# Performance work log

Measured on AMD Instinct MI355X. Metric: run time of the kernel, lower is better.

The kernel has to match this reference:

```python
import jax, jax.numpy as jnp
import numpy as np

N, E, D, L, G = 100000, 300000, 256, 5, 4096


def _bn(x, p):
    # p: [4, dim] = (gamma, beta, running_mean, running_var); eval-mode BatchNorm1d
    g, b, m, v = p
    return (x - m) * jax.lax.rsqrt(v + 1e-5) * g + b


def setup_inputs() -> dict:
    key = jax.random.key(0)
    ks = iter(jax.random.split(key, 48))

    def nrm(shape, scale=0.02):
        return jax.random.normal(next(ks), shape, dtype=jnp.float32) * scale

    def bn_params(n, dim):
        g = 1.0 + nrm((n, dim), 0.1)
        b = nrm((n, dim), 0.1)
        m = nrm((n, dim), 0.1)
        v = 1.0 + jax.random.uniform(next(ks), (n, dim), dtype=jnp.float32)
        return jnp.stack([g, b, m, v], axis=1)  # [n,4,dim]

    return {
        "x": jax.random.randint(next(ks), (N, 9), 0, 2, dtype=jnp.int32),
        "edge_index": jax.random.randint(next(ks), (2, E), 0, N, dtype=jnp.int32),
        "edge_attr": jax.random.randint(next(ks), (E, 3), 0, 2, dtype=jnp.int32),
        "batch": jnp.sort(jax.random.randint(next(ks), (N,), 0, G, dtype=jnp.int32)),
        "atom_emb": nrm((9, 120, D)),            # AtomEncoder: 9 feature tables
        "bond_emb": nrm((L, 3, 6, D)),           # per-layer BondEncoder: 3 feature tables
        "vn0": jnp.zeros((D,), jnp.float32),     # virtualnode embedding (init 0)
        "eps": jnp.zeros((L,), jnp.float32),     # GIN eps per layer
        "conv_W1": nrm((L, D, 2 * D), 1.0 / np.sqrt(D)),     # GIN MLP (sampled BayesLinear)
        "conv_b1": nrm((L, 2 * D)),
        "conv_bn1": bn_params(L, 2 * D),
        "conv_W2": nrm((L, 2 * D, D), 1.0 / np.sqrt(2 * D)),
        "conv_b2": nrm((L, D)),
        "node_bn": bn_params(L, D),              # per-layer outer BatchNorm
        "vn_W1": nrm((L - 1, D, D), 1.0 / np.sqrt(D)),       # virtual-node MLP
        "vn_b1": nrm((L - 1, D)),
        "vn_bn1": bn_params(L - 1, D),
        "vn_W2": nrm((L - 1, D, D), 1.0 / np.sqrt(D)),
        "vn_b2": nrm((L - 1, D)),
        "vn_bn2": bn_params(L - 1, D),
    }


def reference(x, edge_index, edge_attr, batch, atom_emb, bond_emb, vn0, eps,
              conv_W1, conv_b1, conv_bn1, conv_W2, conv_b2, node_bn,
              vn_W1, vn_b1, vn_bn1, vn_W2, vn_b2, vn_bn2):
    src, dst = edge_index[0], edge_index[1]
    n_nodes = x.shape[0]
    n_layers = conv_W1.shape[0]
    # AtomEncoder: sum of 9 feature embeddings -> [N, D]
    h = atom_emb[jnp.arange(9), x].sum(axis=1)
    vn = jnp.broadcast_to(vn0, (G, vn0.shape[0]))  # [G, D]
    for l in range(n_layers):
        # broadcast virtual node into graph's nodes
        h = h + vn[batch]
        # GINConv: msg = relu(x_j + bond_emb), sum-aggregate, MLP((1+eps)x + aggr)
        e = bond_emb[l][jnp.arange(3), edge_attr].sum(axis=1)  # [E, D]
        msg = jax.nn.relu(h[src] + e)
        aggr = jax.ops.segment_sum(msg, dst, num_segments=n_nodes)
        t = (1.0 + eps[l]) * h + aggr
        t = jax.nn.relu(_bn(t @ conv_W1[l] + conv_b1[l], conv_bn1[l])) @ conv_W2[l] + conv_b2[l]
        hn = _bn(t, node_bn[l])  # outer BatchNorm (eval); dropout is identity in eval
        if l < n_layers - 1:
            hn = jax.nn.relu(hn)
            # global_add_pool of pre-conv h, then virtual-node MLP update
            vtemp = jax.ops.segment_sum(h, batch, num_segments=G) + vn
            u = jax.nn.relu(_bn(vtemp @ vn_W1[l] + vn_b1[l], vn_bn1[l]))
            vn = jax.nn.relu(_bn(u @ vn_W2[l] + vn_b2[l], vn_bn2[l]))
        h = hn
    return h  # JK == 'last'
```

## Files before the change

kernel.cpp:

```cpp
#include <hip/hip_runtime.h>

#define NN 100000
#define EE 300000
#define DD 256
#define LL 5
#define GG 4096
#define DB 512
#define MPAD 100096

typedef __attribute__((ext_vector_type(4))) float f32x4;
typedef __attribute__((ext_vector_type(8))) short s16x8;

__device__ __forceinline__ ushort f2bf(float f) {
  unsigned u = __float_as_uint(f);
  return (ushort)((u + 0x7fffu + ((u >> 16) & 1u)) >> 16);
}
__device__ __forceinline__ float b2f(ushort u) {
  return __uint_as_float(((unsigned)u) << 16);
}

__device__ __forceinline__ void gload16(const void* g, void* l) {
  __builtin_amdgcn_global_load_lds((const __attribute__((address_space(1))) void*)g,
                                   (__attribute__((address_space(3))) void*)l, 16, 0, 0);
}

__global__ void k_atom(const int* __restrict__ x, const float* __restrict__ emb,
                       ushort* __restrict__ hb) {
  int n = blockIdx.x * 4 + (threadIdx.x >> 6);
  if (n >= NN) return;
  int d = (threadIdx.x & 63) * 4;
  float ax = 0.f, ay = 0.f, az = 0.f, aw = 0.f;
#pragma unroll
  for (int f = 0; f < 9; ++f) {
    int v = x[n * 9 + f];
    const float4 t = *(const float4*)&emb[((size_t)(f * 120 + v)) * DD + d];
    ax += t.x; ay += t.y; az += t.z; aw += t.w;
  }
  ushort4 o; o.x = f2bf(ax); o.y = f2bf(ay); o.z = f2bf(az); o.w = f2bf(aw);
  *(ushort4*)&hb[(size_t)n * DD + d] = o;
}

__global__ void k_vninit(const float* __restrict__ vn0, float* __restrict__ vn) {
  int i = blockIdx.x * blockDim.x + threadIdx.x;
  if (i < GG * DD) vn[i] = vn0[i & (DD - 1)];
}

__global__ void k_goff(const int* __restrict__ batch, int* __restrict__ goff) {
  int g = blockIdx.x * blockDim.x + threadIdx.x;
  if (g > GG) return;
  if (g == GG) { goff[GG] = NN; return; }
  int lo = 0, hi = NN;
  while (lo < hi) { int mid = (lo + hi) >> 1; if (batch[mid] < g) lo = mid + 1; else hi = mid; }
  goff[g] = lo;
}

__global__ void k_zero(int* __restrict__ p, int n) {
  int i = blockIdx.x * 256 + threadIdx.x;
  if (i < n) p[i] = 0;
}

__global__ void k_deg(const int* __restrict__ dst, int* __restrict__ deg) {
  int e = blockIdx.x * 256 + threadIdx.x;
  if (e < EE) atomicAdd(&deg[dst[e]], 1);
}

__global__ void k_scan1(const int* __restrict__ deg, int* __restrict__ coff,
                        int* __restrict__ bsum) {
  __shared__ int wsum[16];
  __shared__ int wpre[16];
  int lane = threadIdx.x & 63, wid = threadIdx.x >> 6;
  int i = blockIdx.x * 1024 + threadIdx.x;
  int v = (i < NN) ? deg[i] : 0;
  int xv = v;
#pragma unroll
  for (int off = 1; off < 64; off <<= 1) {
    int y = __shfl_up(xv, off);
    if (lane >= off) xv += y;
  }
  if (lane == 63) wsum[wid] = xv;
  __syncthreads();
  if (wid == 0 && lane < 16) {
    int s = wsum[lane];
    int xx = s;
#pragma unroll
    for (int off = 1; off < 16; off <<= 1) {
      int y = __shfl_up(xx, off);
      if (lane >= off) xx += y;
    }
    wpre[lane] = xx - s;
  }
  __syncthreads();
  int val = xv + wpre[wid];
  if (i < NN) coff[i + 1] = val;
  if (threadIdx.x == 1023) bsum[blockIdx.x] = val;
}

__global__ void k_scan2(int* __restrict__ bsum, int nb) {
  __shared__ int ws[2];
  int t = threadIdx.x, lane = t & 63, wid = t >> 6;
  int v = (t < nb) ? bsum[t] : 0;
  int xv = v;
#pragma unroll
  for (int off = 1; off < 64; off <<= 1) {
    int y = __shfl_up(xv, off);
    if (lane >= off) xv += y;
  }
  if (lane == 63) ws[wid] = xv;
  __syncthreads();
  int incl = xv + ((wid == 1) ? ws[0] : 0);
  if (t < nb) bsum[t] = incl - v;
}

__global__ void k_scan3(int* __restrict__ coff, const int* __restrict__ bpre) {
  int i = blockIdx.x * 1024 + threadIdx.x;
  if (i == 0) coff[0] = 0;
  if (i < NN) coff[i + 1] += bpre[i >> 10];
}

__global__ void k_eposinit(const int* __restrict__ coff, int* __restrict__ epos) {
  int n = blockIdx.x * 256 + threadIdx.x;
  if (n < NN) epos[n] = coff[n];
}

__global__ void k_scatter(const int* __restrict__ dst, int* __restrict__ epos,
                          int* __restrict__ eid) {
  int e = blockIdx.x * 256 + threadIdx.x;
  if (e < EE) { int p = atomicAdd(&epos[dst[e]], 1); eid[p] = e; }
}

__global__ void k_sort(const int* __restrict__ coff, int* __restrict__ eid) {
  int n = blockIdx.x * 256 + threadIdx.x;
  if (n >= NN) return;
  int s = coff[n], t = coff[n + 1];
  for (int i = s + 1; i < t; ++i) {
    int key = eid[i]; int j = i - 1;
    while (j >= s && eid[j] > key) { eid[j + 1] = eid[j]; --j; }
    eid[j + 1] = key;
  }
}

__global__ void k_emeta(const int* __restrict__ eid, const int* __restrict__ srcs,
                        const int* __restrict__ eattr, unsigned* __restrict__ emeta) {
  int idx = blockIdx.x * 256 + threadIdx.x;
  if (idx >= EE) return;
  int e = eid[idx];
  int s = srcs[e];
  unsigned c = (unsigned)(eattr[e * 3 + 0] + 2 * eattr[e * 3 + 1] + 4 * eattr[e * 3 + 2]);
  emeta[idx] = (unsigned)s | (c << 17);
}

__global__ void k_bond8(const float* __restrict__ bondE, float* __restrict__ bond8) {
  int l = blockIdx.x, c = blockIdx.y, d = threadIdx.x;
  float v = bondE[(((size_t)l * 3 + 0) * 6 + (c & 1)) * DD + d]
          + bondE[(((size_t)l * 3 + 1) * 6 + ((c >> 1) & 1)) * DD + d]
          + bondE[(((size_t)l * 3 + 2) * 6 + ((c >> 2) & 1)) * DD + d];
  bond8[((size_t)l * 8 + c) * DD + d] = v;
}

__global__ void k_wt(const float* __restrict__ in, ushort* __restrict__ out, int K, int N) {
  __shared__ float t[16][17];
  int l = blockIdx.z;
  int kb = blockIdx.x * 16, nb = blockIdx.y * 16;
  int tx = threadIdx.x & 15, ty = threadIdx.x >> 4;
  t[ty][tx] = in[(size_t)l * K * N + (size_t)(kb + ty) * N + nb + tx];
  __syncthreads();
  out[(size_t)l * N * K + (size_t)(nb + ty) * K + kb + tx] = f2bf(t[tx][ty]);
}

__global__ void k_prep(const ushort* __restrict__ hb, const float* __restrict__ vn,
                       ushort* __restrict__ hvb, ushort* __restrict__ vtempb,
                       const int* __restrict__ goff, int writePool) {
  int g = blockIdx.x * 4 + (threadIdx.x >> 6);
  if (g >= GG) return;
  int d = (threadIdx.x & 63) * 4;
  float4 v = *(const float4*)&vn[(size_t)g * DD + d];
  float ax = v.x, ay = v.y, az = v.z, aw = v.w;
  int r0 = goff[g], r1 = goff[g + 1];
  for (int r = r0; r < r1; ++r) {
    ushort4 hu = *(const ushort4*)&hb[(size_t)r * DD + d];
    float h0 = b2f(hu.x) + v.x, h1 = b2f(hu.y) + v.y;
    float h2 = b2f(hu.z) + v.z, h3 = b2f(hu.w) + v.w;
    ushort4 o; o.x = f2bf(h0); o.y = f2bf(h1); o.z = f2bf(h2); o.w = f2bf(h3);
    *(ushort4*)&hvb[(size_t)r * DD + d] = o;
    ax += h0; ay += h1; az += h2; aw += h3;
  }
  if (writePool) {
    ushort4 o; o.x = f2bf(ax); o.y = f2bf(ay); o.z = f2bf(az); o.w = f2bf(aw);
    *(ushort4*)&vtempb[(size_t)g * DD + d] = o;
  }
}

__global__ void k_aggr(const ushort* __restrict__ hvb, ushort* __restrict__ tb,
                       const unsigned* __restrict__ emeta, const int* __restrict__ coff,
                       const float* __restrict__ bond8l, const float* __restrict__ epsp,
                       int l) {
  int n = blockIdx.x * 4 + (threadIdx.x >> 6);
  if (n >= NN) return;
  int d = (threadIdx.x & 63) * 4;
  float ax = 0.f, ay = 0.f, az = 0.f, aw = 0.f;
  int s0 = coff[n], s1 = coff[n + 1];
  int idx = s0;
  for (; idx + 2 <= s1; idx += 2) {
    unsigned m0 = emeta[idx], m1 = emeta[idx + 1];
    const ushort4 h0 = *(const ushort4*)&hvb[(size_t)(m0 & 0x1FFFFu) * DD + d];
    const ushort4 h1 = *(const ushort4*)&hvb[(size_t)(m1 & 0x1FFFFu) * DD + d];
    const float4 b0 = *(const float4*)&bond8l[(size_t)(m0 >> 17) * DD + d];
    const float4 b1 = *(const float4*)&bond8l[(size_t)(m1 >> 17) * DD + d];
    ax += fmaxf(b2f(h0.x) + b0.x, 0.f) + fmaxf(b2f(h1.x) + b1.x, 0.f);
    ay += fmaxf(b2f(h0.y) + b0.y, 0.f) + fmaxf(b2f(h1.y) + b1.y, 0.f);
    az += fmaxf(b2f(h0.z) + b0.z, 0.f) + fmaxf(b2f(h1.z) + b1.z, 0.f);
    aw += fmaxf(b2f(h0.w) + b0.w, 0.f) + fmaxf(b2f(h1.w) + b1.w, 0.f);
  }
  if (idx < s1) {
    unsigned m0 = emeta[idx];
    const ushort4 h0 = *(const ushort4*)&hvb[(size_t)(m0 & 0x1FFFFu) * DD + d];
    const float4 b0 = *(const float4*)&bond8l[(size_t)(m0 >> 17) * DD + d];
    ax += fmaxf(b2f(h0.x) + b0.x, 0.f);
    ay += fmaxf(b2f(h0.y) + b0.y, 0.f);
    az += fmaxf(b2f(h0.z) + b0.z, 0.f);
    aw += fmaxf(b2f(h0.w) + b0.w, 0.f);
  }
  float ep = 1.f + epsp[l];
  const ushort4 hn = *(const ushort4*)&hvb[(size_t)n * DD + d];
  ushort4 o;
  o.x = f2bf(ep * b2f(hn.x) + ax); o.y = f2bf(ep * b2f(hn.y) + ay);
  o.z = f2bf(ep * b2f(hn.z) + az); o.w = f2bf(ep * b2f(hn.w) + aw);
  *(ushort4*)&tb[(size_t)n * DD + d] = o;
}

__global__ __launch_bounds__(256) void k_mfma_gemm(
    const ushort* __restrict__ A, int M, int K,
    const ushort* __restrict__ BT, int N,
    void* __restrict__ Cv, int outBf16, int doRelu,
    const float* __restrict__ bias, const float* __restrict__ bn) {
  __shared__ ushort Asm[2][128 * 32];
  __shared__ ushort Bsm[2][128 * 32];
  const int tid = threadIdx.x;
  const int lane = tid & 63;
  const int w = tid >> 6;
  const int rowBase = blockIdx.x * 128;
  const int colBase = blockIdx.y * 128;
  const int wrow = (w >> 1) * 64, wcol = (w & 1) * 64;
  const int r16 = lane & 15, kgrp = lane >> 4;

  f32x4 acc[4][4];
#pragma unroll
  for (int m = 0; m < 4; ++m)
#pragma unroll
    for (int n = 0; n < 4; ++n) acc[m][n] = (f32x4)0.f;

  const int ca0 = tid, ca1 = tid + 256;
  const int ra0 = ca0 >> 2, ka0 = (ca0 & 3) ^ ((ra0 >> 1) & 3);
  const int ra1 = ca1 >> 2, ka1 = (ca1 & 3) ^ ((ra1 >> 1) & 3);
  const ushort* Ap0 = A + (size_t)(rowBase + ra0) * K + ka0 * 8;
  const ushort* Ap1 = A + (size_t)(rowBase + ra1) * K + ka1 * 8;
  const ushort* Bp0 = BT + (size_t)(colBase + ra0) * K + ka0 * 8;
  const ushort* Bp1 = BT + (size_t)(colBase + ra1) * K + ka1 * 8;

  int aoff[4], boff[4];
#pragma unroll
  for (int m = 0; m < 4; ++m) {
    int row = wrow + m * 16 + r16;
    aoff[m] = row * 64 + ((kgrp ^ ((row >> 1) & 3)) << 4);
    int col = wcol + m * 16 + r16;
    boff[m] = col * 64 + ((kgrp ^ ((col >> 1) & 3)) << 4);
  }

  const int nk = K >> 5;
  gload16(Ap0, (char*)Asm + ca0 * 16);
  gload16(Ap1, (char*)Asm + ca1 * 16);
  gload16(Bp0, (char*)Bsm + ca0 * 16);
  gload16(Bp1, (char*)Bsm + ca1 * 16);
  __syncthreads();

  int cur = 0;
  for (int t = 0; t < nk; ++t) {
    int nxt = cur ^ 1;
    if (t + 1 < nk) {
      int ko = (t + 1) << 5;
      gload16(Ap0 + ko, (char*)Asm + nxt * 8192 + ca0 * 16);
      gload16(Ap1 + ko, (char*)Asm + nxt * 8192 + ca1 * 16);
      gload16(Bp0 + ko, (char*)Bsm + nxt * 8192 + ca0 * 16);
      gload16(Bp1 + ko, (char*)Bsm + nxt * 8192 + ca1 * 16);
    }
    const char* cA = (const char*)Asm + cur * 8192;
    const char* cB = (const char*)Bsm + cur * 8192;
    s16x8 a[4], b[4];
#pragma unroll
    for (int m = 0; m < 4; ++m) a[m] = *(const s16x8*)(cA + aoff[m]);
#pragma unroll
    for (int n = 0; n < 4; ++n) b[n] = *(const s16x8*)(cB + boff[n]);
#pragma unroll
    for (int m = 0; m < 4; ++m)
#pragma unroll
      for (int n = 0; n < 4; ++n)
        acc[m][n] = __builtin_amdgcn_mfma_f32_16x16x32_bf16(a[m], b[n], acc[m][n], 0, 0, 0);
    __syncthreads();
    cur = nxt;
  }

  float alpha[4], beta[4];
#pragma unroll
  for (int n = 0; n < 4; ++n) {
    int col = colBase + wcol + n * 16 + r16;
    float g = bn[col], bb = bn[N + col], mm = bn[2 * N + col], vv = bn[3 * N + col];
    float s = g * rsqrtf(vv + 1e-5f);
    alpha[n] = s; beta[n] = fmaf(bias[col] - mm, s, bb);
  }
#pragma unroll
  for (int m = 0; m < 4; ++m) {
#pragma unroll
    for (int r = 0; r < 4; ++r) {
      int row = rowBase + wrow + m * 16 + kgrp * 4 + r;
      if (row < M) {
#pragma unroll
        for (int n = 0; n < 4; ++n) {
          int col = colBase + wcol + n * 16 + r16;
          float v = fmaf(acc[m][n][r], alpha[n], beta[n]);
          if (doRelu) v = fmaxf(v, 0.f);
          if (outBf16) ((ushort*)Cv)[(size_t)row * N + col] = f2bf(v);
          else         ((float*)Cv)[(size_t)row * N + col] = v;
        }
      }
    }
  }
}

extern "C" void kernel_launch(void* const* d_in, const int* in_sizes, int n_in,
                              void* d_out, int out_size, void* d_ws, size_t ws_size,
                              hipStream_t stream) {
  const int*   x     = (const int*)d_in[0];
  const int*   ei    = (const int*)d_in[1];
  const int*   ea    = (const int*)d_in[2];
  const int*   batch = (const int*)d_in[3];
  const float* atomE = (const float*)d_in[4];
  const float* bondE = (const float*)d_in[5];
  const float* vn0   = (const float*)d_in[6];
  const float* eps   = (const float*)d_in[7];
  const float* cW1   = (const float*)d_in[8];
  const float* cb1   = (const float*)d_in[9];
  const float* cbn1  = (const float*)d_in[10];
  const float* cW2   = (const float*)d_in[11];
  const float* cb2   = (const float*)d_in[12];
  const float* nbn   = (const float*)d_in[13];
  const float* vW1   = (const float*)d_in[14];
  const float* vb1   = (const float*)d_in[15];
  const float* vbn1  = (const float*)d_in[16];
  const float* vW2   = (const float*)d_in[17];
  const float* vb2   = (const float*)d_in[18];
  const float* vbn2  = (const float*)d_in[19];
  (void)in_sizes; (void)n_in; (void)out_size; (void)ws_size;

  char* wsp = (char*)d_ws;
  size_t o = 0;
  auto alloc = [&](size_t bytes) -> char* {
    char* p = wsp + o; o += (bytes + 255) & ~(size_t)255; return p;
  };
  ushort* tbuf  = (ushort*)alloc((size_t)MPAD * DD * 2);
  ushort* c1b   = (ushort*)alloc((size_t)MPAD * DB * 2);
  ushort* hb    = (ushort*)alloc((size_t)NN * DD * 2);
  float*  vn    = (float*) alloc((size_t)GG * DD * 4);
  ushort* vtmpb = (ushort*)alloc((size_t)GG * DD * 2);
  ushort* ub    = (ushort*)alloc((size_t)GG * DD * 2);
  ushort* bw1   = (ushort*)alloc((size_t)LL * DB * DD * 2);
  ushort* bw2   = (ushort*)alloc((size_t)LL * DD * DB * 2);
  ushort* bvw1  = (ushort*)alloc((size_t)(LL - 1) * DD * DD * 2);
  ushort* bvw2  = (ushort*)alloc((size_t)(LL - 1) * DD * DD * 2);
  float*  bond8 = (float*) alloc((size_t)LL * 8 * DD * 4);
  unsigned* emeta = (unsigned*)alloc((size_t)EE * 4);
  int* coff = (int*)alloc((size_t)(NN + 1) * 4);
  int* deg  = (int*)alloc((size_t)NN * 4);
  int* epos = (int*)alloc((size_t)NN * 4);
  int* eid  = (int*)alloc((size_t)EE * 4);
  int* goff = (int*)alloc((size_t)(GG + 1) * 4);
  int* bsum = (int*)alloc((size_t)128 * 4);

  const int* srcs = ei;
  const int* dsts = ei + EE;
  ushort* hvb = (ushort*)d_out;

  k_atom<<<(NN + 3) / 4, 256, 0, stream>>>(x, atomE, hb);
  k_vninit<<<(GG * DD + 255) / 256, 256, 0, stream>>>(vn0, vn);
  k_goff<<<(GG + 256) / 256, 256, 0, stream>>>(batch, goff);
  k_zero<<<(NN + 255) / 256, 256, 0, stream>>>(deg, NN);
  k_deg<<<(EE + 255) / 256, 256, 0, stream>>>(dsts, deg);
  {
    int nb = (NN + 1023) / 1024;
    k_scan1<<<nb, 1024, 0, stream>>>(deg, coff, bsum);
    k_scan2<<<1, 128, 0, stream>>>(bsum, nb);
    k_scan3<<<nb, 1024, 0, stream>>>(coff, bsum);
  }
  k_eposinit<<<(NN + 255) / 256, 256, 0, stream>>>(coff, epos);
  k_scatter<<<(EE + 255) / 256, 256, 0, stream>>>(dsts, epos, eid);
  k_sort<<<(NN + 255) / 256, 256, 0, stream>>>(coff, eid);
  k_emeta<<<(EE + 255) / 256, 256, 0, stream>>>(eid, srcs, ea, emeta);
  k_bond8<<<dim3(LL, 8), 256, 0, stream>>>(bondE, bond8);
  k_wt<<<dim3(DD / 16, DB / 16, LL), 256, 0, stream>>>(cW1, bw1, DD, DB);
  k_wt<<<dim3(DB / 16, DD / 16, LL), 256, 0, stream>>>(cW2, bw2, DB, DD);
  k_wt<<<dim3(DD / 16, DD / 16, LL - 1), 256, 0, stream>>>(vW1, bvw1, DD, DD);
  k_wt<<<dim3(DD / 16, DD / 16, LL - 1), 256, 0, stream>>>(vW2, bvw2, DD, DD);

  for (int l = 0; l < LL; ++l) {
    int writePool = (l < LL - 1) ? 1 : 0;
    k_prep<<<(GG + 3) / 4, 256, 0, stream>>>(hb, vn, hvb, vtmpb, goff, writePool);
    k_aggr<<<(NN + 3) / 4, 256, 0, stream>>>(hvb, tbuf, emeta, coff,
                                             bond8 + (size_t)l * 8 * DD, eps, l);
    k_mfma_gemm<<<dim3(MPAD / 128, DB / 128), 256, 0, stream>>>(
        tbuf, NN, DD, bw1 + (size_t)l * DB * DD, DB,
        c1b, 1, 1, cb1 + (size_t)l * DB, cbn1 + (size_t)l * 4 * DB);
    if (l < LL - 1) {
      k_mfma_gemm<<<dim3(MPAD / 128, DD / 128), 256, 0, stream>>>(
          c1b, NN, DB, bw2 + (size_t)l * DD * DB, DD,
          hb, 1, 1, cb2 + (size_t)l * DD, nbn + (size_t)l * 4 * DD);
      k_mfma_gemm<<<dim3(GG / 128, DD / 128), 256, 0, stream>>>(
          vtmpb, GG, DD, bvw1 + (size_t)l * DD * DD, DD,
          ub, 1, 1, vb1 + (size_t)l * DD, vbn1 + (size_t)l * 4 * DD);
      k_mfma_gemm<<<dim3(GG / 128, DD / 128), 256, 0, stream>>>(
          ub, GG, DD, bvw2 + (size_t)l * DD * DD, DD,
          vn, 0, 1, vb2 + (size_t)l * DD, vbn2 + (size_t)l * 4 * DD);
    } else {
      k_mfma_gemm<<<dim3(MPAD / 128, DD / 128), 256, 0, stream>>>(
          c1b, NN, DB, bw2 + (size_t)l * DD * DB, DD,
          (float*)d_out, 0, 0, cb2 + (size_t)l * DD, nbn + (size_t)l * 4 * DD);
    }
  }
}
```

Baseline: 1.154 ms.

## Fuse virtual-node broadcast into GEMM epilogue and keep full A row-tile in LDS

Removes the per-layer prep pass that re-read h and wrote h+vn. The virtual node is instead added in the atom encoder for layer 0 and in the second GIN GEMM's epilogue, after the virtual-node MLP has been reordered to run first. Pooling becomes a read-only kernel over the already-broadcast h. The GEMM is rewritten as a template that loads the whole A row tile (all of K) into LDS once and sweeps every output column chunk, streaming B double-buffered, so A is fetched from global memory only once. The trade-offs are much higher LDS use per block (fewer resident blocks), a per-row batch gather in the epilogue, and a serial loop over column chunks inside one block.

```diff
diff --git a/kernel.cpp b/kernel.cpp
--- a/kernel.cpp
+++ b/kernel.cpp
@@ -25,11 +25,12 @@
 }
 
 __global__ void k_atom(const int* __restrict__ x, const float* __restrict__ emb,
-                       ushort* __restrict__ hb) {
+                       const float* __restrict__ vn0, ushort* __restrict__ hvb) {
   int n = blockIdx.x * 4 + (threadIdx.x >> 6);
   if (n >= NN) return;
   int d = (threadIdx.x & 63) * 4;
-  float ax = 0.f, ay = 0.f, az = 0.f, aw = 0.f;
+  const float4 v0 = *(const float4*)&vn0[d];
+  float ax = v0.x, ay = v0.y, az = v0.z, aw = v0.w;
 #pragma unroll
   for (int f = 0; f < 9; ++f) {
     int v = x[n * 9 + f];
@@ -37,7 +38,7 @@
     ax += t.x; ay += t.y; az += t.z; aw += t.w;
   }
   ushort4 o; o.x = f2bf(ax); o.y = f2bf(ay); o.z = f2bf(az); o.w = f2bf(aw);
-  *(ushort4*)&hb[(size_t)n * DD + d] = o;
+  *(ushort4*)&hvb[(size_t)n * DD + d] = o;
 }
 
 __global__ void k_vninit(const float* __restrict__ vn0, float* __restrict__ vn) {
@@ -167,9 +168,8 @@
   out[(size_t)l * N * K + (size_t)(nb + ty) * K + kb + tx] = f2bf(t[tx][ty]);
 }
 
-__global__ void k_prep(const ushort* __restrict__ hb, const float* __restrict__ vn,
-                       ushort* __restrict__ hvb, ushort* __restrict__ vtempb,
-                       const int* __restrict__ goff, int writePool) {
+__global__ void k_pool(const ushort* __restrict__ hvb, const float* __restrict__ vn,
+                       ushort* __restrict__ vtempb, const int* __restrict__ goff) {
   int g = blockIdx.x * 4 + (threadIdx.x >> 6);
   if (g >= GG) return;
   int d = (threadIdx.x & 63) * 4;
@@ -177,17 +177,11 @@
   float ax = v.x, ay = v.y, az = v.z, aw = v.w;
   int r0 = goff[g], r1 = goff[g + 1];
   for (int r = r0; r < r1; ++r) {
-    ushort4 hu = *(const ushort4*)&hb[(size_t)r * DD + d];
-    float h0 = b2f(hu.x) + v.x, h1 = b2f(hu.y) + v.y;
-    float h2 = b2f(hu.z) + v.z, h3 = b2f(hu.w) + v.w;
-    ushort4 o; o.x = f2bf(h0); o.y = f2bf(h1); o.z = f2bf(h2); o.w = f2bf(h3);
-    *(ushort4*)&hvb[(size_t)r * DD + d] = o;
-    ax += h0; ay += h1; az += h2; aw += h3;
-  }
-  if (writePool) {
-    ushort4 o; o.x = f2bf(ax); o.y = f2bf(ay); o.z = f2bf(az); o.w = f2bf(aw);
-    *(ushort4*)&vtempb[(size_t)g * DD + d] = o;
-  }
+    ushort4 hu = *(const ushort4*)&hvb[(size_t)r * DD + d];
+    ax += b2f(hu.x); ay += b2f(hu.y); az += b2f(hu.z); aw += b2f(hu.w);
+  }
+  ushort4 o; o.x = f2bf(ax); o.y = f2bf(ay); o.z = f2bf(az); o.w = f2bf(aw);
+  *(ushort4*)&vtempb[(size_t)g * DD + d] = o;
 }
 
 __global__ void k_aggr(const ushort* __restrict__ hvb, ushort* __restrict__ tb,
@@ -228,101 +222,117 @@
   *(ushort4*)&tb[(size_t)n * DD + d] = o;
 }
 
-__global__ __launch_bounds__(256) void k_mfma_gemm(
-    const ushort* __restrict__ A, int M, int K,
-    const ushort* __restrict__ BT, int N,
+template<int TM, int K, int NT>
+__global__ __launch_bounds__(256) void k_gemm_f(
+    const ushort* __restrict__ A, int M,
+    const ushort* __restrict__ BT,
     void* __restrict__ Cv, int outBf16, int doRelu,
-    const float* __restrict__ bias, const float* __restrict__ bn) {
-  __shared__ ushort Asm[2][128 * 32];
-  __shared__ ushort Bsm[2][128 * 32];
+    const float* __restrict__ bias, const float* __restrict__ bn,
+    const float* __restrict__ vnAdd, const int* __restrict__ batchv) {
+  constexpr int KS = K / 8;
+  constexpr int NK = K / 32;
+  constexpr int NC = NT / 128;
+  constexpr int MF = TM / 32;
+  __shared__ ushort Alds[TM * K];
+  __shared__ ushort Blds[2][128 * 32];
   const int tid = threadIdx.x;
   const int lane = tid & 63;
   const int w = tid >> 6;
-  const int rowBase = blockIdx.x * 128;
-  const int colBase = blockIdx.y * 128;
-  const int wrow = (w >> 1) * 64, wcol = (w & 1) * 64;
+  const int rowBase = blockIdx.x * TM;
+  const int wrow = (w >> 1) * (TM / 2);
+  const int wcol = (w & 1) * 64;
   const int r16 = lane & 15, kgrp = lane >> 4;
 
-  f32x4 acc[4][4];
-#pragma unroll
-  for (int m = 0; m < 4; ++m)
+#pragma unroll
+  for (int i = 0; i < TM * KS / 256; ++i) {
+    int c = tid + i * 256;
+    int row = c / KS, s = c % KS;
+    int kg = s ^ (row & 7);
+    gload16(A + (size_t)(rowBase + row) * K + kg * 8, (char*)Alds + c * 16);
+  }
+  const int bcol0 = tid >> 2, bkg0 = (tid & 3) ^ ((bcol0 >> 1) & 3);
+  const int bcol1 = (tid + 256) >> 2, bkg1 = ((tid + 256) & 3) ^ ((bcol1 >> 1) & 3);
+  auto stageB = [&](int pc, int pt, int b) {
+    const ushort* base = BT + (size_t)pc * 128 * K + pt * 32;
+    gload16(base + (size_t)bcol0 * K + bkg0 * 8, (char*)Blds[b] + tid * 16);
+    gload16(base + (size_t)bcol1 * K + bkg1 * 8, (char*)Blds[b] + (tid + 256) * 16);
+  };
+  stageB(0, 0, 0);
+  __syncthreads();
+
+  int rbyte[MF], x7[MF];
+#pragma unroll
+  for (int m = 0; m < MF; ++m) {
+    int row = wrow + m * 16 + r16;
+    rbyte[m] = row * KS * 16;
+    x7[m] = row & 7;
+  }
+  int boff[4];
+#pragma unroll
+  for (int n = 0; n < 4; ++n) {
+    int col = wcol + n * 16 + r16;
+    boff[n] = (col * 4 + (kgrp ^ ((col >> 1) & 3))) * 16;
+  }
+
+  f32x4 acc[MF][4];
+#pragma unroll
+  for (int m = 0; m < MF; ++m)
 #pragma unroll
     for (int n = 0; n < 4; ++n) acc[m][n] = (f32x4)0.f;
 
-  const int ca0 = tid, ca1 = tid + 256;
-  const int ra0 = ca0 >> 2, ka0 = (ca0 & 3) ^ ((ra0 >> 1) & 3);
-  const int ra1 = ca1 >> 2, ka1 = (ca1 & 3) ^ ((ra1 >> 1) & 3);
-  const ushort* Ap0 = A + (size_t)(rowBase + ra0) * K + ka0 * 8;
-  const ushort* Ap1 = A + (size_t)(rowBase + ra1) * K + ka1 * 8;
-  const ushort* Bp0 = BT + (size_t)(colBase + ra0) * K + ka0 * 8;
-  const ushort* Bp1 = BT + (size_t)(colBase + ra1) * K + ka1 * 8;
-
-  int aoff[4], boff[4];
-#pragma unroll
-  for (int m = 0; m < 4; ++m) {
-    int row = wrow + m * 16 + r16;
-    aoff[m] = row * 64 + ((kgrp ^ ((row >> 1) & 3)) << 4);
-    int col = wcol + m * 16 + r16;
-    boff[m] = col * 64 + ((kgrp ^ ((col >> 1) & 3)) << 4);
-  }
-
-  const int nk = K >> 5;
-  gload16(Ap0, (char*)Asm + ca0 * 16);
-  gload16(Ap1, (char*)Asm + ca1 * 16);
-  gload16(Bp0, (char*)Bsm + ca0 * 16);
-  gload16(Bp1, (char*)Bsm + ca1 * 16);
-  __syncthreads();
-
   int cur = 0;
-  for (int t = 0; t < nk; ++t) {
-    int nxt = cur ^ 1;
-    if (t + 1 < nk) {
-      int ko = (t + 1) << 5;
-      gload16(Ap0 + ko, (char*)Asm + nxt * 8192 + ca0 * 16);
-      gload16(Ap1 + ko, (char*)Asm + nxt * 8192 + ca1 * 16);
-      gload16(Bp0 + ko, (char*)Bsm + nxt * 8192 + ca0 * 16);
-      gload16(Bp1 + ko, (char*)Bsm + nxt * 8192 + ca1 * 16);
-    }
-    const char* cA = (const char*)Asm + cur * 8192;
-    const char* cB = (const char*)Bsm + cur * 8192;
-    s16x8 a[4], b[4];
-#pragma unroll
-    for (int m = 0; m < 4; ++m) a[m] = *(const s16x8*)(cA + aoff[m]);
-#pragma unroll
-    for (int n = 0; n < 4; ++n) b[n] = *(const s16x8*)(cB + boff[n]);
-#pragma unroll
-    for (int m = 0; m < 4; ++m)
+  for (int c = 0; c < NC; ++c) {
+#pragma unroll
+    for (int t = 0; t < NK; ++t) {
+      if (t + 1 < NK) stageB(c, t + 1, cur ^ 1);
+      else if (c + 1 < NC) stageB(c + 1, 0, cur ^ 1);
+      s16x8 a[MF], b[4];
+#pragma unroll
+      for (int m = 0; m < MF; ++m)
+        a[m] = *(const s16x8*)((const char*)Alds + rbyte[m] + ((((t << 2) + kgrp) ^ x7[m]) << 4));
 #pragma unroll
       for (int n = 0; n < 4; ++n)
-        acc[m][n] = __builtin_amdgcn_mfma_f32_16x16x32_bf16(a[m], b[n], acc[m][n], 0, 0, 0);
-    __syncthreads();
-    cur = nxt;
-  }
-
-  float alpha[4], beta[4];
-#pragma unroll
-  for (int n = 0; n < 4; ++n) {
-    int col = colBase + wcol + n * 16 + r16;
-    float g = bn[col], bb = bn[N + col], mm = bn[2 * N + col], vv = bn[3 * N + col];
-    float s = g * rsqrtf(vv + 1e-5f);
-    alpha[n] = s; beta[n] = fmaf(bias[col] - mm, s, bb);
-  }
-#pragma unroll
-  for (int m = 0; m < 4; ++m) {
-#pragma unroll
-    for (int r = 0; r < 4; ++r) {
-      int row = rowBase + wrow + m * 16 + kgrp * 4 + r;
-      if (row < M) {
-#pragma unroll
-        for (int n = 0; n < 4; ++n) {
-          int col = colBase + wcol + n * 16 + r16;
-          float v = fmaf(acc[m][n][r], alpha[n], beta[n]);
-          if (doRelu) v = fmaxf(v, 0.f);
-          if (outBf16) ((ushort*)Cv)[(size_t)row * N + col] = f2bf(v);
-          else         ((float*)Cv)[(size_t)row * N + col] = v;
+        b[n] = *(const s16x8*)((const char*)Blds[cur] + boff[n]);
+#pragma unroll
+      for (int m = 0; m < MF; ++m)
+#pragma unroll
+        for (int n = 0; n < 4; ++n)
+          acc[m][n] = __builtin_amdgcn_mfma_f32_16x16x32_bf16(a[m], b[n], acc[m][n], 0, 0, 0);
+      __syncthreads();
+      cur ^= 1;
+    }
+    const int cb = c * 128;
+    float alpha[4], beta[4];
+#pragma unroll
+    for (int n = 0; n < 4; ++n) {
+      int col = cb + wcol + n * 16 + r16;
+      float g = bn[col], bb = bn[NT + col], mm = bn[2 * NT + col], vv = bn[3 * NT + col];
+      float s = g * rsqrtf(vv + 1e-5f);
+      alpha[n] = s; beta[n] = fmaf(bias[col] - mm, s, bb);
+    }
+#pragma unroll
+    for (int m = 0; m < MF; ++m) {
+#pragma unroll
+      for (int r = 0; r < 4; ++r) {
+        int row = rowBase + wrow + m * 16 + kgrp * 4 + r;
+        if (row < M) {
+          const float* vp = vnAdd ? (vnAdd + (size_t)batchv[row] * NT) : nullptr;
+#pragma unroll
+          for (int n = 0; n < 4; ++n) {
+            int col = cb + wcol + n * 16 + r16;
+            float v = fmaf(acc[m][n][r], alpha[n], beta[n]);
+            if (doRelu) v = fmaxf(v, 0.f);
+            if (vp) v += vp[col];
+            if (outBf16) ((ushort*)Cv)[(size_t)row * NT + col] = f2bf(v);
+            else         ((float*)Cv)[(size_t)row * NT + col] = v;
+          }
         }
       }
     }
+#pragma unroll
+    for (int m = 0; m < MF; ++m)
+#pragma unroll
+      for (int n = 0; n < 4; ++n) acc[m][n] = (f32x4)0.f;
   }
 }
 
@@ -358,7 +368,6 @@
   };
   ushort* tbuf  = (ushort*)alloc((size_t)MPAD * DD * 2);
   ushort* c1b   = (ushort*)alloc((size_t)MPAD * DB * 2);
-  ushort* hb    = (ushort*)alloc((size_t)NN * DD * 2);
   float*  vn    = (float*) alloc((size_t)GG * DD * 4);
   ushort* vtmpb = (ushort*)alloc((size_t)GG * DD * 2);
   ushort* ub    = (ushort*)alloc((size_t)GG * DD * 2);
@@ -379,7 +388,7 @@
   const int* dsts = ei + EE;
   ushort* hvb = (ushort*)d_out;
 
-  k_atom<<<(NN + 3) / 4, 256, 0, stream>>>(x, atomE, hb);
+  k_atom<<<(NN + 3) / 4, 256, 0, stream>>>(x, atomE, vn0, hvb);
   k_vninit<<<(GG * DD + 255) / 256, 256, 0, stream>>>(vn0, vn);
   k_goff<<<(GG + 256) / 256, 256, 0, stream>>>(batch, goff);
   k_zero<<<(NN + 255) / 256, 256, 0, stream>>>(deg, NN);
@@ -401,27 +410,28 @@
   k_wt<<<dim3(DD / 16, DD / 16, LL - 1), 256, 0, stream>>>(vW2, bvw2, DD, DD);
 
   for (int l = 0; l < LL; ++l) {
-    int writePool = (l < LL - 1) ? 1 : 0;
-    k_prep<<<(GG + 3) / 4, 256, 0, stream>>>(hb, vn, hvb, vtmpb, goff, writePool);
+    if (l < LL - 1) {
+      k_pool<<<(GG + 3) / 4, 256, 0, stream>>>(hvb, vn, vtmpb, goff);
+      k_gemm_f<64, 256, 256><<<GG / 64, 256, 0, stream>>>(
+          vtmpb, GG, bvw1 + (size_t)l * DD * DD, ub, 1, 1,
+          vb1 + (size_t)l * DD, vbn1 + (size_t)l * 4 * DD, nullptr, nullptr);
+      k_gemm_f<64, 256, 256><<<GG / 64, 256, 0, stream>>>(
+          ub, GG, bvw2 + (size_t)l * DD * DD, vn, 0, 1,
+          vb2 + (size_t)l * DD, vbn2 + (size_t)l * 4 * DD, nullptr, nullptr);
+    }
     k_aggr<<<(NN + 3) / 4, 256, 0, stream>>>(hvb, tbuf, emeta, coff,
                                              bond8 + (size_t)l * 8 * DD, eps, l);
-    k_mfma_gemm<<<dim3(MPAD / 128, DB / 128), 256, 0, stream>>>(
-        tbuf, NN, DD, bw1 + (size_t)l * DB * DD, DB,
-        c1b, 1, 1, cb1 + (size_t)l * DB, cbn1 + (size_t)l * 4 * DB);
+    k_gemm_f<128, 256, 512><<<MPAD / 128, 256, 0, stream>>>(
+        tbuf, NN, bw1 + (size_t)l * DB * DD, c1b, 1, 1,
+        cb1 + (size_t)l * DB, cbn1 + (size_t)l * 4 * DB, nullptr, nullptr);
     if (l < LL - 1) {
-      k_mfma_gemm<<<dim3(MPAD / 128, DD / 128), 256, 0, stream>>>(
-          c1b, NN, DB, bw2 + (size_t)l * DD * DB, DD,
-          hb, 1, 1, cb2 + (size_t)l * DD, nbn + (size_t)l * 4 * DD);
-      k_mfma_gemm<<<dim3(GG / 128, DD / 128), 256, 0, stream>>>(
-          vtmpb, GG, DD, bvw1 + (size_t)l * DD * DD, DD,
-          ub, 1, 1, vb1 + (size_t)l * DD, vbn1 + (size_t)l * 4 * DD);
-      k_mfma_gemm<<<dim3(GG / 128, DD / 128), 256, 0, stream>>>(
-          ub, GG, DD, bvw2 + (size_t)l * DD * DD, DD,
-          vn, 0, 1, vb2 + (size_t)l * DD, vbn2 + (size_t)l * 4 * DD);
+      k_gemm_f<64, 512, 256><<<MPAD / 64, 256, 0, stream>>>(
+          c1b, NN, bw2 + (size_t)l * DD * DB, hvb, 1, 1,
+          cb2 + (size_t)l * DD, nbn + (size_t)l * 4 * DD, vn, batch);
     } else {
-      k_mfma_gemm<<<dim3(MPAD / 128, DD / 128), 256, 0, stream>>>(
-          c1b, NN, DB, bw2 + (size_t)l * DD * DB, DD,
-          (float*)d_out, 0, 0, cb2 + (size_t)l * DD, nbn + (size_t)l * 4 * DD);
-    }
-  }
-}
+      k_gemm_f<64, 512, 256><<<MPAD / 64, 256, 0, stream>>>(
+          c1b, NN, bw2 + (size_t)l * DD * DB, (float*)d_out, 0, 0,
+          cb2 + (size_t)l * DD, nbn + (size_t)l * 4 * DD, nullptr, nullptr);
+    }
+  }
+}
```

New measurement: 1.398 ms. +21.2%, slower.

## Fuse virtual-node broadcast into GEMM epilogue and add XCD-aware block remap

Applied to the files above, without the earlier changes.

The per-layer prep pass that added the virtual node to every node row is removed. Instead, the virtual-node MLP now runs before aggregation, and the second conv GEMM's epilogue adds vn[batch[row]] while writing the next layer's hvb. The atom encoder also folds in vn0 directly. This removes one full read/write pass over the node feature matrix per layer, at the cost of an extra gathered load per output row in the GEMM epilogue. The GEMM also switches to a 1D grid with an XCD-aware block index remap, meant to improve L2 locality across chiplets.

```diff
diff --git a/kernel.cpp b/kernel.cpp
--- a/kernel.cpp
+++ b/kernel.cpp
@@ -25,11 +25,12 @@
 }
 
 __global__ void k_atom(const int* __restrict__ x, const float* __restrict__ emb,
-                       ushort* __restrict__ hb) {
+                       const float* __restrict__ vn0, ushort* __restrict__ hvb) {
   int n = blockIdx.x * 4 + (threadIdx.x >> 6);
   if (n >= NN) return;
   int d = (threadIdx.x & 63) * 4;
-  float ax = 0.f, ay = 0.f, az = 0.f, aw = 0.f;
+  const float4 v0 = *(const float4*)&vn0[d];
+  float ax = v0.x, ay = v0.y, az = v0.z, aw = v0.w;
 #pragma unroll
   for (int f = 0; f < 9; ++f) {
     int v = x[n * 9 + f];
@@ -37,7 +38,7 @@
     ax += t.x; ay += t.y; az += t.z; aw += t.w;
   }
   ushort4 o; o.x = f2bf(ax); o.y = f2bf(ay); o.z = f2bf(az); o.w = f2bf(aw);
-  *(ushort4*)&hb[(size_t)n * DD + d] = o;
+  *(ushort4*)&hvb[(size_t)n * DD + d] = o;
 }
 
 __global__ void k_vninit(const float* __restrict__ vn0, float* __restrict__ vn) {
@@ -167,9 +168,8 @@
   out[(size_t)l * N * K + (size_t)(nb + ty) * K + kb + tx] = f2bf(t[tx][ty]);
 }
 
-__global__ void k_prep(const ushort* __restrict__ hb, const float* __restrict__ vn,
-                       ushort* __restrict__ hvb, ushort* __restrict__ vtempb,
-                       const int* __restrict__ goff, int writePool) {
+__global__ void k_pool(const ushort* __restrict__ hvb, const float* __restrict__ vn,
+                       ushort* __restrict__ vtempb, const int* __restrict__ goff) {
   int g = blockIdx.x * 4 + (threadIdx.x >> 6);
   if (g >= GG) return;
   int d = (threadIdx.x & 63) * 4;
@@ -177,17 +177,11 @@
   float ax = v.x, ay = v.y, az = v.z, aw = v.w;
   int r0 = goff[g], r1 = goff[g + 1];
   for (int r = r0; r < r1; ++r) {
-    ushort4 hu = *(const ushort4*)&hb[(size_t)r * DD + d];
-    float h0 = b2f(hu.x) + v.x, h1 = b2f(hu.y) + v.y;
-    float h2 = b2f(hu.z) + v.z, h3 = b2f(hu.w) + v.w;
-    ushort4 o; o.x = f2bf(h0); o.y = f2bf(h1); o.z = f2bf(h2); o.w = f2bf(h3);
-    *(ushort4*)&hvb[(size_t)r * DD + d] = o;
-    ax += h0; ay += h1; az += h2; aw += h3;
-  }
-  if (writePool) {
-    ushort4 o; o.x = f2bf(ax); o.y = f2bf(ay); o.z = f2bf(az); o.w = f2bf(aw);
-    *(ushort4*)&vtempb[(size_t)g * DD + d] = o;
-  }
+    ushort4 hu = *(const ushort4*)&hvb[(size_t)r * DD + d];
+    ax += b2f(hu.x); ay += b2f(hu.y); az += b2f(hu.z); aw += b2f(hu.w);
+  }
+  ushort4 o; o.x = f2bf(ax); o.y = f2bf(ay); o.z = f2bf(az); o.w = f2bf(aw);
+  *(ushort4*)&vtempb[(size_t)g * DD + d] = o;
 }
 
 __global__ void k_aggr(const ushort* __restrict__ hvb, ushort* __restrict__ tb,
@@ -230,17 +224,23 @@
 
 __global__ __launch_bounds__(256) void k_mfma_gemm(
     const ushort* __restrict__ A, int M, int K,
-    const ushort* __restrict__ BT, int N,
+    const ushort* __restrict__ BT, int N, int CT,
     void* __restrict__ Cv, int outBf16, int doRelu,
-    const float* __restrict__ bias, const float* __restrict__ bn) {
+    const float* __restrict__ bias, const float* __restrict__ bn,
+    const float* __restrict__ vnAdd, const int* __restrict__ batchv) {
   __shared__ ushort Asm[2][128 * 32];
   __shared__ ushort Bsm[2][128 * 32];
+  const int T = gridDim.x;
+  const int q = T >> 3, r = T & 7;
+  const int xcd = blockIdx.x & 7, li = blockIdx.x >> 3;
+  const int w0 = xcd * q + (xcd < r ? xcd : r) + li;
+  const int rowBase = (w0 / CT) * 128;
+  const int colBase = (w0 % CT) * 128;
+
   const int tid = threadIdx.x;
   const int lane = tid & 63;
-  const int w = tid >> 6;
-  const int rowBase = blockIdx.x * 128;
-  const int colBase = blockIdx.y * 128;
-  const int wrow = (w >> 1) * 64, wcol = (w & 1) * 64;
+  const int wv = tid >> 6;
+  const int wrow = (wv >> 1) * 64, wcol = (wv & 1) * 64;
   const int r16 = lane & 15, kgrp = lane >> 4;
 
   f32x4 acc[4][4];
@@ -310,14 +310,16 @@
 #pragma unroll
   for (int m = 0; m < 4; ++m) {
 #pragma unroll
-    for (int r = 0; r < 4; ++r) {
-      int row = rowBase + wrow + m * 16 + kgrp * 4 + r;
+    for (int rr = 0; rr < 4; ++rr) {
+      int row = rowBase + wrow + m * 16 + kgrp * 4 + rr;
       if (row < M) {
+        const float* vp = vnAdd ? (vnAdd + (size_t)batchv[row] * N) : nullptr;
 #pragma unroll
         for (int n = 0; n < 4; ++n) {
           int col = colBase + wcol + n * 16 + r16;
-          float v = fmaf(acc[m][n][r], alpha[n], beta[n]);
+          float v = fmaf(acc[m][n][rr], alpha[n], beta[n]);
           if (doRelu) v = fmaxf(v, 0.f);
+          if (vp) v += vp[col];
           if (outBf16) ((ushort*)Cv)[(size_t)row * N + col] = f2bf(v);
           else         ((float*)Cv)[(size_t)row * N + col] = v;
         }
@@ -358,7 +360,6 @@
   };
   ushort* tbuf  = (ushort*)alloc((size_t)MPAD * DD * 2);
   ushort* c1b   = (ushort*)alloc((size_t)MPAD * DB * 2);
-  ushort* hb    = (ushort*)alloc((size_t)NN * DD * 2);
   float*  vn    = (float*) alloc((size_t)GG * DD * 4);
   ushort* vtmpb = (ushort*)alloc((size_t)GG * DD * 2);
   ushort* ub    = (ushort*)alloc((size_t)GG * DD * 2);
@@ -379,7 +380,7 @@
   const int* dsts = ei + EE;
   ushort* hvb = (ushort*)d_out;
 
-  k_atom<<<(NN + 3) / 4, 256, 0, stream>>>(x, atomE, hb);
+  k_atom<<<(NN + 3) / 4, 256, 0, stream>>>(x, atomE, vn0, hvb);
   k_vninit<<<(GG * DD + 255) / 256, 256, 0, stream>>>(vn0, vn);
   k_goff<<<(GG + 256) / 256, 256, 0, stream>>>(batch, goff);
   k_zero<<<(NN + 255) / 256, 256, 0, stream>>>(deg, NN);
@@ -401,27 +402,29 @@
   k_wt<<<dim3(DD / 16, DD / 16, LL - 1), 256, 0, stream>>>(vW2, bvw2, DD, DD);
 
   for (int l = 0; l < LL; ++l) {
-    int writePool = (l < LL - 1) ? 1 : 0;
-    k_prep<<<(GG + 3) / 4, 256, 0, stream>>>(hb, vn, hvb, vtmpb, goff, writePool);
+    if (l < LL - 1) {
+      k_pool<<<(GG + 3) / 4, 256, 0, stream>>>(hvb, vn, vtmpb, goff);
+      k_mfma_gemm<<<(GG / 128) * 2, 256, 0, stream>>>(
+          vtmpb, GG, DD, bvw1 + (size_t)l * DD * DD, DD, 2,
+          ub, 1, 1, vb1 + (size_t)l * DD, vbn1 + (size_t)l * 4 * DD, nullptr, nullptr);
+      k_mfma_gemm<<<(GG / 128) * 2, 256, 0, stream>>>(
+          ub, GG, DD, bvw2 + (size_t)l * DD * DD, DD, 2,
+          vn, 0, 1, vb2 + (size_t)l * DD, vbn2 + (size_t)l * 4 * DD, nullptr, nullptr);
+    }
     k_aggr<<<(NN + 3) / 4, 256, 0, stream>>>(hvb, tbuf, emeta, coff,
                                              bond8 + (size_t)l * 8 * DD, eps, l);
-    k_mfma_gemm<<<dim3(MPAD / 128, DB / 128), 256, 0, stream>>>(
-        tbuf, NN, DD, bw1 + (size_t)l * DB * DD, DB,
-        c1b, 1, 1, cb1 + (size_t)l * DB, cbn1 + (size_t)l * 4 * DB);
+    k_mfma_gemm<<<(MPAD / 128) * 4, 256, 0, stream>>>(
+        tbuf, NN, DD, bw1 + (size_t)l * DB * DD, DB, 4,
+        c1b, 1, 1, cb1 + (size_t)l * DB, cbn1 + (size_t)l * 4 * DB, nullptr, nullptr);
     if (l < LL - 1) {
-      k_mfma_gemm<<<dim3(MPAD / 128, DD / 128), 256, 0, stream>>>(
-          c1b, NN, DB, bw2 + (size_t)l * DD * DB, DD,
-          hb, 1, 1, cb2 + (size_t)l * DD, nbn + (size_t)l * 4 * DD);
-      k_mfma_gemm<<<dim3(GG / 128, DD / 128), 256, 0, stream>>>(
-          vtmpb, GG, DD, bvw1 + (size_t)l * DD * DD, DD,
-          ub, 1, 1, vb1 + (size_t)l * DD, vbn1 + (size_t)l * 4 * DD);
-      k_mfma_gemm<<<dim3(GG / 128, DD / 128), 256, 0, stream>>>(
-          ub, GG, DD, bvw2 + (size_t)l * DD * DD, DD,
-          vn, 0, 1, vb2 + (size_t)l * DD, vbn2 + (size_t)l * 4 * DD);
+      k_mfma_gemm<<<(MPAD / 128) * 2, 256, 0, stream>>>(
+          c1b, NN, DB, bw2 + (size_t)l * DD * DB, DD, 2,
+          hvb, 1, 1, cb2 + (size_t)l * DD, nbn + (size_t)l * 4 * DD, vn, batch);
     } else {
-      k_mfma_gemm<<<dim3(MPAD / 128, DD / 128), 256, 0, stream>>>(
-          c1b, NN, DB, bw2 + (size_t)l * DD * DB, DD,
-          (float*)d_out, 0, 0, cb2 + (size_t)l * DD, nbn + (size_t)l * 4 * DD);
+      k_mfma_gemm<<<(MPAD / 128) * 2, 256, 0, stream>>>(
+          c1b, NN, DB, bw2 + (size_t)l * DD * DB, DD, 2,
+          (float*)d_out, 0, 0, cb2 + (size_t)l * DD, nbn + (size_t)l * 4 * DD,
+          nullptr, nullptr);
     }
   }
 }
```

Measured after the change: 1.160 ms. Within noise of the previous version (+0.5%).
